# Kernel optimization log

Measured on AMD Instinct MI355X. Metric: run time of the kernel, lower is better.

Reference implementation:

```python
import jax, jax.numpy as jnp
import numpy as np


def setup_inputs() -> dict:
    key = jax.random.key(0)
    images = jax.random.uniform(key, (64, 384, 384, 3), dtype=jnp.float32)
    return {"images": images, "k": 5}


def reference(images, k):
    # cv2.dilate with a k x k kernel of ones == per-channel max filter with SAME padding.
    # Applied over the whole batch in one fused reduce_window (window only over H, W).
    out = jax.lax.reduce_window(
        images,
        -jnp.inf,
        jax.lax.max,
        window_dimensions=(1, k, k, 1),
        window_strides=(1, 1, 1, 1),
        padding="SAME",
    )
    # cv_to_tf appends a trailing singleton dim before tf.stack -> (B, H, W, C, 1)
    return out[..., None]
```

## Files before the change

kernel.cpp:

```cpp
#include <hip/hip_runtime.h>


#define Bn 64
#define H 384
#define ROWF 1152
#define ROWBYTES (ROWF * 4)
#define WF4 288
#define RB 12
#define NLOAD (RB + 4)
#define GROUPS 8
#define STRIPS 5
#define SOUT 60
#define NBLK (Bn * GROUPS * STRIPS)
#define NEGINF (-3.402823466e+38f)

typedef float f32x4 __attribute__((ext_vector_type(4)));

__device__ __forceinline__ float4 max4(float4 a, float4 b) {
  return make_float4(fmaxf(a.x, b.x), fmaxf(a.y, b.y),
                     fmaxf(a.z, b.z), fmaxf(a.w, b.w));
}
__device__ __forceinline__ float4 shflup4(float4 v, int d) {
  return make_float4(__shfl_up(v.x, d), __shfl_up(v.y, d),
                     __shfl_up(v.z, d), __shfl_up(v.w, d));
}
__device__ __forceinline__ float4 shfldn4(float4 v, int d) {
  return make_float4(__shfl_down(v.x, d), __shfl_down(v.y, d),
                     __shfl_down(v.z, d), __shfl_down(v.w, d));
}

__global__ __launch_bounds__(256, 4) void dilate5_kernel(
    const float* __restrict__ in, float* __restrict__ out) {
  const int wv = threadIdx.x >> 6;
  const int lane = threadIdx.x & 63;

  const int orig = blockIdx.x;
  int t = (orig & 7) * (NBLK / 8) + (orig >> 3);
  const int strip = t % STRIPS; t /= STRIPS;
  const int grp = t % GROUPS;   t /= GROUPS;
  const int b = t;

  const int row0 = (grp * 4 + wv) * RB;
  const int col = strip * SOUT - 2 + lane;
  const bool cvalid = (col >= 0) && (col < WF4);
  const int ccl = col < 0 ? 0 : (col > WF4 - 1 ? WF4 - 1 : col);
  const size_t coff = (size_t)ccl * 16;
  const bool willstore = (lane >= 2) && (lane < 62) && (col < WF4);

  const float4 ninf = make_float4(NEGINF, NEGINF, NEGINF, NEGINF);
  const char* __restrict__ imgb = (const char*)in + (size_t)b * H * ROWBYTES;
  char* __restrict__ outb = (char*)out + (size_t)b * H * ROWBYTES;

  float4 raw[NLOAD];
#pragma unroll
  for (int j = 0; j < NLOAD; ++j) {
    int gh = row0 - 2 + j;
    int ghc = gh < 0 ? 0 : (gh > H - 1 ? H - 1 : gh);
    raw[j] = *reinterpret_cast<const float4*>(imgb + (size_t)ghc * ROWBYTES + coff);
  }

  if (row0 == 0)      { raw[0] = ninf; raw[1] = ninf; }
  if (row0 == H - RB) { raw[NLOAD - 2] = ninf; raw[NLOAD - 1] = ninf; }

#pragma unroll
  for (int i = 0; i < RB; ++i) {
    const int o = row0 + i;
    float4 v = max4(max4(max4(raw[i], raw[i + 1]), max4(raw[i + 2], raw[i + 3])),
                    raw[i + 4]);
    if (!cvalid) v = ninf;

    float4 A = shflup4(v, 2);
    float4 Bv = shflup4(v, 1);
    float4 D = shfldn4(v, 1);
    float4 E = shfldn4(v, 2);
    float4 h;
    h.x = fmaxf(fmaxf(fmaxf(A.z, Bv.y), fmaxf(v.x, v.w)), D.z);
    h.y = fmaxf(fmaxf(fmaxf(A.w, Bv.z), fmaxf(v.y, D.x)), D.w);
    h.z = fmaxf(fmaxf(fmaxf(Bv.x, Bv.w), fmaxf(v.z, D.y)), E.x);
    h.w = fmaxf(fmaxf(fmaxf(Bv.y, v.x), fmaxf(v.w, D.z)), E.y);

    if (willstore) {
      f32x4 hv; hv.x = h.x; hv.y = h.y; hv.z = h.z; hv.w = h.w;
      __builtin_nontemporal_store(
          hv, reinterpret_cast<f32x4*>(outb + (size_t)o * ROWBYTES + coff));
    }
  }
}

extern "C" void kernel_launch(void* const* d_in, const int* in_sizes, int n_in,
                              void* d_out, int out_size, void* d_ws, size_t ws_size,
                              hipStream_t stream) {
  const float* images = (const float*)d_in[0];
  float* out = (float*)d_out;
  dilate5_kernel<<<NBLK, 256, 0, stream>>>(images, out);
}
```

Measured before the change: 204.2 us.

## Double rows per wave and stream row loads with a rolling prefetch

Each wave now produces 24 output rows instead of 12, which cuts the redundant halo-row reads per output. Rows are no longer all loaded up front: an 8-row prefetch window is refilled inside the compute loop. This is meant to lower register pressure, so the launch-bounds occupancy hint rises from 4 to 5. Shuffles whose results were never used are dropped, and the explicit -inf top/bottom padding is removed in favour of row clamping, which gives the same max. Risks are fewer blocks in total and less memory-level parallelism per wave from the shallower prefetch.

```diff
diff --git a/kernel.cpp b/kernel.cpp
--- a/kernel.cpp
+++ b/kernel.cpp
@@ -6,12 +6,13 @@
 #define ROWF 1152
 #define ROWBYTES (ROWF * 4)
 #define WF4 288
-#define RB 12
+#define RB 24
 #define NLOAD (RB + 4)
-#define GROUPS 8
+#define PF 8
+#define CHUNKS 4
 #define STRIPS 5
 #define SOUT 60
-#define NBLK (Bn * GROUPS * STRIPS)
+#define NBLK (Bn * STRIPS * CHUNKS)
 #define NEGINF (-3.402823466e+38f)
 
 typedef float f32x4 __attribute__((ext_vector_type(4)));
@@ -29,7 +30,7 @@
                      __shfl_down(v.z, d), __shfl_down(v.w, d));
 }
 
-__global__ __launch_bounds__(256, 4) void dilate5_kernel(
+__global__ __launch_bounds__(256, 5) void dilate5_kernel(
     const float* __restrict__ in, float* __restrict__ out) {
   const int wv = threadIdx.x >> 6;
   const int lane = threadIdx.x & 63;
@@ -37,10 +38,10 @@
   const int orig = blockIdx.x;
   int t = (orig & 7) * (NBLK / 8) + (orig >> 3);
   const int strip = t % STRIPS; t /= STRIPS;
-  const int grp = t % GROUPS;   t /= GROUPS;
+  const int chunk = t % CHUNKS; t /= CHUNKS;
   const int b = t;
 
-  const int row0 = (grp * 4 + wv) * RB;
+  const int r0 = (chunk * 4 + wv) * RB;
   const int col = strip * SOUT - 2 + lane;
   const bool cvalid = (col >= 0) && (col < WF4);
   const int ccl = col < 0 ? 0 : (col > WF4 - 1 ? WF4 - 1 : col);
@@ -51,38 +52,39 @@
   const char* __restrict__ imgb = (const char*)in + (size_t)b * H * ROWBYTES;
   char* __restrict__ outb = (char*)out + (size_t)b * H * ROWBYTES;
 
+  auto loadrow = [&](int gh) -> float4 {
+    int ghc = gh < 0 ? 0 : (gh > H - 1 ? H - 1 : gh);
+    return *reinterpret_cast<const float4*>(imgb + (size_t)ghc * ROWBYTES + coff);
+  };
+
   float4 raw[NLOAD];
 #pragma unroll
-  for (int j = 0; j < NLOAD; ++j) {
-    int gh = row0 - 2 + j;
-    int ghc = gh < 0 ? 0 : (gh > H - 1 ? H - 1 : gh);
-    raw[j] = *reinterpret_cast<const float4*>(imgb + (size_t)ghc * ROWBYTES + coff);
-  }
-
-  if (row0 == 0)      { raw[0] = ninf; raw[1] = ninf; }
-  if (row0 == H - RB) { raw[NLOAD - 2] = ninf; raw[NLOAD - 1] = ninf; }
+  for (int j = 0; j < PF; ++j) raw[j] = loadrow(r0 - 2 + j);
 
 #pragma unroll
   for (int i = 0; i < RB; ++i) {
-    const int o = row0 + i;
+    if (i + PF < NLOAD) raw[i + PF] = loadrow(r0 - 2 + i + PF);
+
     float4 v = max4(max4(max4(raw[i], raw[i + 1]), max4(raw[i + 2], raw[i + 3])),
                     raw[i + 4]);
     if (!cvalid) v = ninf;
 
-    float4 A = shflup4(v, 2);
     float4 Bv = shflup4(v, 1);
-    float4 D = shfldn4(v, 1);
-    float4 E = shfldn4(v, 2);
+    float4 D  = shfldn4(v, 1);
+    float Az = __shfl_up(v.z, 2);
+    float Aw = __shfl_up(v.w, 2);
+    float Ex = __shfl_down(v.x, 2);
+    float Ey = __shfl_down(v.y, 2);
     float4 h;
-    h.x = fmaxf(fmaxf(fmaxf(A.z, Bv.y), fmaxf(v.x, v.w)), D.z);
-    h.y = fmaxf(fmaxf(fmaxf(A.w, Bv.z), fmaxf(v.y, D.x)), D.w);
-    h.z = fmaxf(fmaxf(fmaxf(Bv.x, Bv.w), fmaxf(v.z, D.y)), E.x);
-    h.w = fmaxf(fmaxf(fmaxf(Bv.y, v.x), fmaxf(v.w, D.z)), E.y);
+    h.x = fmaxf(fmaxf(fmaxf(Az, Bv.y), fmaxf(v.x, v.w)), D.z);
+    h.y = fmaxf(fmaxf(fmaxf(Aw, Bv.z), fmaxf(v.y, D.x)), D.w);
+    h.z = fmaxf(fmaxf(fmaxf(Bv.x, Bv.w), fmaxf(v.z, D.y)), Ex);
+    h.w = fmaxf(fmaxf(fmaxf(Bv.y, v.x), fmaxf(v.w, D.z)), Ey);
 
     if (willstore) {
       f32x4 hv; hv.x = h.x; hv.y = h.y; hv.z = h.z; hv.w = h.w;
       __builtin_nontemporal_store(
-          hv, reinterpret_cast<f32x4*>(outb + (size_t)o * ROWBYTES + coff));
+          hv, reinterpret_cast<f32x4*>(outb + (size_t)(r0 + i) * ROWBYTES + coff));
     }
   }
 }
```

Result: no change. 205.8 us (+0.8%).
